# Kernel tuning notes

Hardware: AMD Instinct MI355X
Metric: run time of the kernel (lower is better)

Reference implementation:

```python
import jax, jax.numpy as jnp
import numpy as np

IN_DIM = 128
DIM = 32
N_HEADS = 4
EPS = 1e-5


def setup_inputs() -> dict:
    key = jax.random.key(0)
    ks = jax.random.split(key, 8)
    b, L = 1, 320
    s = 0.02
    return {
        "z": jax.random.normal(ks[0], (b, L, L, IN_DIM), dtype=jnp.float32),
        "ln_g": jnp.ones((IN_DIM,), jnp.float32),
        "ln_b": jnp.zeros((IN_DIM,), jnp.float32),
        "Wqkv": jax.random.normal(ks[1], (IN_DIM, DIM * 3 * N_HEADS), jnp.float32) * s,
        "Wpair": jax.random.normal(ks[2], (IN_DIM, N_HEADS), jnp.float32) * s,
        "Wgate": jax.random.normal(ks[3], (IN_DIM, N_HEADS * DIM), jnp.float32) * s,
        "bgate": jnp.zeros((N_HEADS * DIM,), jnp.float32),
        "Wout": jax.random.normal(ks[4], (N_HEADS * DIM, IN_DIM), jnp.float32) * s,
        "bout": jnp.zeros((IN_DIM,), jnp.float32),
    }


def _layernorm(x, g, b):
    m = jnp.mean(x, axis=-1, keepdims=True)
    v = jnp.mean(jnp.square(x - m), axis=-1, keepdims=True)
    return (x - m) * jax.lax.rsqrt(v + EPS) * g + b


def reference(z, ln_g, ln_b, Wqkv, Wpair, Wgate, bgate, Wout, bout):
    B, L, _, _ = z.shape
    zn = _layernorm(z, ln_g, ln_b)  # [b,i,j,c]
    qkv = zn @ Wqkv                 # [b,i,j,3*h*d]
    q, k, v = jnp.split(qkv, 3, axis=-1)
    rs = lambda t: t.reshape(B, L, L, N_HEADS, DIM)
    q, k, v = rs(q), rs(k), rs(v)
    pair_bias = zn @ Wpair          # [b,i,j,h]
    gate = jax.nn.sigmoid(zn @ Wgate + bgate)  # [b,i,j,h*d]
    scale = DIM ** 0.5
    # row-wise: attend over j within each row r=i
    # scores: [b,r,i,j,h]; bias broadcast over r
    scores = jnp.einsum('brihd,brjhd->brijh', q, k / scale)
    scores = scores + pair_bias[:, None]
    attn = jax.nn.softmax(scores, axis=3)
    out = jnp.einsum('brijh,brjhd->brihd', attn, v)  # [b,r,i,h,d]
    out = out.reshape(B, L, L, N_HEADS * DIM)
    return (gate * out) @ Wout + bout
```

## Files before the change

kernel.cpp:

```cpp
#include <hip/hip_runtime.h>
#include <math.h>


#define LL 320
#define CC 128
#define NPOS (LL*LL)

typedef __attribute__((ext_vector_type(8))) __bf16 bf16x8;
typedef __attribute__((ext_vector_type(4))) __bf16 bf16x4;
typedef __attribute__((ext_vector_type(4))) float f32x4;

#define MFMA16(a,b,c) __builtin_amdgcn_mfma_f32_16x16x32_bf16(a,b,c,0,0,0)

__device__ __forceinline__ int swz(int m, int kc) {
    return m*128 + ((kc ^ (m & 7)) << 3);
}

__global__ __launch_bounds__(128) void k_wprep(
    const float* __restrict__ Wqkv, const float* __restrict__ Wgate,
    const float* __restrict__ Wout, __bf16* __restrict__ wT)
{
    const int n = blockIdx.x, t = threadIdx.x;
    float v;
    if (n < 384)      v = Wqkv[(size_t)t*384 + n] * (n < 128 ? 0.17677669529663687f : 1.f);
    else if (n < 512) v = Wgate[(size_t)t*128 + (n-384)];
    else              v = Wout[(size_t)t*128 + (n-512)];
    wT[(size_t)n*128 + t] = (__bf16)v;
}

__global__ __launch_bounds__(512) void k_ln_proj(
    const float* __restrict__ z, const float* __restrict__ lng, const float* __restrict__ lnb,
    const __bf16* __restrict__ wT, const float* __restrict__ Wpair,
    const float* __restrict__ bgate,
    __bf16* __restrict__ qkvb, __bf16* __restrict__ biasb, __bf16* __restrict__ gateb)
{
    __shared__ __bf16 As[128*128];
    __shared__ __bf16 Bs[128*128];
    const int t = threadIdx.x;
    const int posBase = blockIdx.x * 128;

    {
        const int r0 = t >> 2, q = t & 3;
        const float* zp = z + (size_t)(posBase + r0)*CC + q*32;
        float v[32];
        float s = 0.f, sq = 0.f;
#pragma unroll
        for (int i = 0; i < 8; ++i) {
            float4 f = ((const float4*)zp)[i];
            v[4*i+0]=f.x; v[4*i+1]=f.y; v[4*i+2]=f.z; v[4*i+3]=f.w;
            s  += f.x + f.y + f.z + f.w;
            sq += f.x*f.x + f.y*f.y + f.z*f.z + f.w*f.w;
        }
        s  += __shfl_xor(s, 1);  sq += __shfl_xor(sq, 1);
        s  += __shfl_xor(s, 2);  sq += __shfl_xor(sq, 2);
        const float mean = s * (1.f/128.f);
        const float var  = sq * (1.f/128.f) - mean*mean;
        const float rstd = rsqrtf(var + 1e-5f);
        const float4* g4 = (const float4*)(lng + q*32);
        const float4* b4 = (const float4*)(lnb + q*32);
#pragma unroll
        for (int i = 0; i < 8; ++i) {
            float4 gg = g4[i], bb = b4[i];
            v[4*i+0] = (v[4*i+0]-mean)*rstd*gg.x + bb.x;
            v[4*i+1] = (v[4*i+1]-mean)*rstd*gg.y + bb.y;
            v[4*i+2] = (v[4*i+2]-mean)*rstd*gg.z + bb.z;
            v[4*i+3] = (v[4*i+3]-mean)*rstd*gg.w + bb.w;
        }
#pragma unroll
        for (int i2 = 0; i2 < 8; ++i2) {
            bf16x4 pk;
            pk[0] = (__bf16)v[4*i2+0]; pk[1] = (__bf16)v[4*i2+1];
            pk[2] = (__bf16)v[4*i2+2]; pk[3] = (__bf16)v[4*i2+3];
            *(bf16x4*)&As[swz(r0, q*4 + (i2>>1)) + (i2&1)*4] = pk;
        }
        float pc0=0.f, pc1=0.f, pc2=0.f, pc3=0.f;
#pragma unroll 8
        for (int kk = 0; kk < 32; ++kk) {
            float4 wp = *(const float4*)&Wpair[(q*32 + kk)*4];
            pc0 += v[kk]*wp.x; pc1 += v[kk]*wp.y; pc2 += v[kk]*wp.z; pc3 += v[kk]*wp.w;
        }
        pc0 += __shfl_xor(pc0,1); pc0 += __shfl_xor(pc0,2);
        pc1 += __shfl_xor(pc1,1); pc1 += __shfl_xor(pc1,2);
        pc2 += __shfl_xor(pc2,1); pc2 += __shfl_xor(pc2,2);
        pc3 += __shfl_xor(pc3,1); pc3 += __shfl_xor(pc3,2);
        if (q == 0) {
            biasb[0*(size_t)NPOS + posBase + r0] = (__bf16)pc0;
            biasb[1*(size_t)NPOS + posBase + r0] = (__bf16)pc1;
            biasb[2*(size_t)NPOS + posBase + r0] = (__bf16)pc2;
            biasb[3*(size_t)NPOS + posBase + r0] = (__bf16)pc3;
        }
    }

    const int lane = t & 63, wv = t >> 6;
    const int l15 = lane & 15, quad = lane >> 4;
    const int m0 = wv * 16;
    const int srow = t >> 2, skc0 = (t & 3) * 4;

    for (int ch = 0; ch < 4; ++ch) {
        __syncthreads();
        {
            const __bf16* src = wT + (size_t)(ch*128 + srow)*128;
#pragma unroll
            for (int j = 0; j < 4; ++j)
                *(bf16x8*)&Bs[swz(srow, skc0 + j)] = *(const bf16x8*)(src + (skc0 + j)*8);
        }
        __syncthreads();

        f32x4 acc[8] = {};
#pragma unroll
        for (int kstep = 0; kstep < 4; ++kstep) {
            bf16x8 aA = *(const bf16x8*)&As[swz(m0 + l15, kstep*4 + quad)];
#pragma unroll
            for (int nt = 0; nt < 8; ++nt) {
                bf16x8 bB = *(const bf16x8*)&Bs[swz(nt*16 + l15, kstep*4 + quad)];
                acc[nt] = MFMA16(aA, bB, acc[nt]);
            }
        }

        if (ch < 3) {
#pragma unroll
            for (int reg = 0; reg < 4; ++reg) {
                __bf16* qp = qkvb + (size_t)(posBase + m0 + quad*4 + reg)*384 + ch*128 + l15;
#pragma unroll
                for (int nt = 0; nt < 8; ++nt)
                    qp[nt*16] = (__bf16)acc[nt][reg];
            }
        } else {
#pragma unroll
            for (int reg = 0; reg < 4; ++reg) {
                __bf16* gp = gateb + (size_t)(posBase + m0 + quad*4 + reg)*128 + l15;
#pragma unroll
                for (int nt = 0; nt < 8; ++nt) {
                    float x = acc[nt][reg] + bgate[nt*16 + l15];
                    gp[nt*16] = (__bf16)(1.f/(1.f + __expf(-x)));
                }
            }
        }
    }
}

#define KS_ST 40
#define VT_ST 328
#define PW_ST 40
__global__ __launch_bounds__(320) void k_attn(
    const __bf16* __restrict__ qkvb, const __bf16* __restrict__ biasb,
    const __bf16* __restrict__ gateb, __bf16* __restrict__ attb)
{
    __shared__ __bf16 Ks[320*KS_ST];
    __shared__ __bf16 Vt[32*VT_ST];
    __shared__ __bf16 Pw[5*64*PW_ST];

    const int t = threadIdx.x, wave = t / 64, lane = t & 63;
    const int l15 = lane & 15, quad = lane >> 4;
    const int r = blockIdx.x, h = blockIdx.y;
    const int i0 = wave * 64;
    const size_t rowBase = (size_t)r * LL;

    {
        const __bf16* kp = qkvb + (rowBase + t)*384 + 128 + h*32;
#pragma unroll
        for (int c = 0; c < 4; ++c)
            *(bf16x8*)&Ks[t*KS_ST + c*8] = *(const bf16x8*)(kp + c*8);
#pragma unroll
        for (int c = 0; c < 4; ++c) {
            bf16x8 vv = *(const bf16x8*)(kp + 128 + c*8);
#pragma unroll
            for (int e = 0; e < 8; ++e)
                Vt[(c*8 + e)*VT_ST + t] = vv[e];
        }
    }

    bf16x8 qf[4];
#pragma unroll
    for (int nt = 0; nt < 4; ++nt)
        qf[nt] = *(const bf16x8*)(qkvb + (rowBase + i0 + nt*16 + l15)*384 + h*32 + quad*8);

    __syncthreads();

    f32x4 O[4][2] = {};
    float lp[4] = {0.f,0.f,0.f,0.f};
    __bf16* pw = &Pw[wave*64*PW_ST];
    const __bf16* bbase = biasb + (size_t)h*NPOS;

    for (int j0 = 0; j0 < LL; j0 += 32) {
        const f32x4 zero = {0.f,0.f,0.f,0.f};
        bf16x8 kf[2];
#pragma unroll
        for (int mt = 0; mt < 2; ++mt)
            kf[mt] = *(const bf16x8*)&Ks[(j0 + mt*16 + l15)*KS_ST + quad*8];
        f32x4 st[2][4];
#pragma unroll
        for (int mt = 0; mt < 2; ++mt)
#pragma unroll
            for (int nt = 0; nt < 4; ++nt)
                st[mt][nt] = MFMA16(kf[mt], qf[nt], zero);

#pragma unroll
        for (int nt = 0; nt < 4; ++nt) {
            const size_t bi = (size_t)(i0 + nt*16 + l15)*LL + j0;
#pragma unroll
            for (int mt = 0; mt < 2; ++mt) {
                bf16x4 bb = *(const bf16x4*)(bbase + bi + mt*16 + quad*4);
                bf16x4 pk;
                float rs = 0.f;
#pragma unroll
                for (int reg = 0; reg < 4; ++reg) {
                    float p = __expf(st[mt][nt][reg] + (float)bb[reg]);
                    pk[reg] = (__bf16)p;
                    rs += p;
                }
                lp[nt] += rs;
                *(bf16x4*)&pw[(nt*16 + l15)*PW_ST + mt*16 + quad*4] = pk;
            }
        }

        bf16x8 vf[2];
#pragma unroll
        for (int dt = 0; dt < 2; ++dt)
            vf[dt] = *(const bf16x8*)&Vt[(dt*16 + l15)*VT_ST + j0 + quad*8];
#pragma unroll
        for (int nt = 0; nt < 4; ++nt) {
            bf16x8 pf = *(const bf16x8*)&pw[(nt*16 + l15)*PW_ST + quad*8];
#pragma unroll
            for (int dt = 0; dt < 2; ++dt)
                O[nt][dt] = MFMA16(pf, vf[dt], O[nt][dt]);
        }
    }

#pragma unroll
    for (int nt = 0; nt < 4; ++nt) {
        lp[nt] += __shfl_xor(lp[nt], 16);
        lp[nt] += __shfl_xor(lp[nt], 32);
    }
#pragma unroll
    for (int nt = 0; nt < 4; ++nt) {
#pragma unroll
        for (int reg = 0; reg < 4; ++reg) {
            const float lsum = __shfl(lp[nt], quad*4 + reg);
            const float inv = 1.f / lsum;
            const size_t pos = rowBase + i0 + nt*16 + quad*4 + reg;
#pragma unroll
            for (int dt = 0; dt < 2; ++dt) {
                const int d = dt*16 + l15;
                const float g = (float)gateb[pos*128 + h*32 + d];
                attb[pos*128 + h*32 + d] = (__bf16)(O[nt][dt][reg] * inv * g);
            }
        }
    }
}

__global__ __launch_bounds__(512) void k_out(
    const __bf16* __restrict__ attb, const __bf16* __restrict__ wT,
    const float* __restrict__ bout, float* __restrict__ out)
{
    __shared__ __bf16 As[128*128];
    __shared__ __bf16 Bs[128*128];
    const int t = threadIdx.x;
    const int posBase = blockIdx.x * 128;
    const int srow = t >> 2, skc0 = (t & 3) * 4;

    {
        const __bf16* asrc = attb + (size_t)(posBase + srow)*128;
        const __bf16* bsrc = wT + (size_t)(512 + srow)*128;
#pragma unroll
        for (int j = 0; j < 4; ++j) {
            *(bf16x8*)&As[swz(srow, skc0 + j)] = *(const bf16x8*)(asrc + (skc0 + j)*8);
            *(bf16x8*)&Bs[swz(srow, skc0 + j)] = *(const bf16x8*)(bsrc + (skc0 + j)*8);
        }
    }
    __syncthreads();

    const int lane = t & 63, wv = t >> 6;
    const int l15 = lane & 15, quad = lane >> 4;
    const int m0 = wv * 16;

    f32x4 acc[8] = {};
#pragma unroll
    for (int kstep = 0; kstep < 4; ++kstep) {
        bf16x8 aA = *(const bf16x8*)&As[swz(m0 + l15, kstep*4 + quad)];
#pragma unroll
        for (int nt = 0; nt < 8; ++nt) {
            bf16x8 bB = *(const bf16x8*)&Bs[swz(nt*16 + l15, kstep*4 + quad)];
            acc[nt] = MFMA16(aA, bB, acc[nt]);
        }
    }

#pragma unroll
    for (int reg = 0; reg < 4; ++reg) {
        float* op = out + (size_t)(posBase + m0 + quad*4 + reg)*128 + l15;
#pragma unroll
        for (int nt = 0; nt < 8; ++nt)
            op[nt*16] = acc[nt][reg] + bout[nt*16 + l15];
    }
}

extern "C" void kernel_launch(void* const* d_in, const int* in_sizes, int n_in,
                              void* d_out, int out_size, void* d_ws, size_t ws_size,
                              hipStream_t stream) {
    const float* z     = (const float*)d_in[0];
    const float* ln_g  = (const float*)d_in[1];
    const float* ln_b  = (const float*)d_in[2];
    const float* Wqkv  = (const float*)d_in[3];
    const float* Wpair = (const float*)d_in[4];
    const float* Wgate = (const float*)d_in[5];
    const float* bgate = (const float*)d_in[6];
    const float* Wout  = (const float*)d_in[7];
    const float* bout  = (const float*)d_in[8];
    float* out = (float*)d_out;

    __bf16* qkvb  = (__bf16*)d_ws;
    __bf16* attb  = qkvb  + (size_t)NPOS*384;
    __bf16* wT    = attb  + (size_t)NPOS*128;
    __bf16* gateb = wT    + (size_t)640*128;
    __bf16* biasb = gateb + (size_t)NPOS*128;

    k_wprep<<<640, 128, 0, stream>>>(Wqkv, Wgate, Wout, wT);
    k_ln_proj<<<800, 512, 0, stream>>>(z, ln_g, ln_b, wT, Wpair, bgate, qkvb, biasb, gateb);
    k_attn<<<dim3(320, 4), 320, 0, stream>>>(qkvb, biasb, gateb, attb);
    k_out<<<800, 512, 0, stream>>>(attb, wT, bout, out);
}
```

Before: 295.0 us.

## Pre-swizzle pair bias, fold log2e, stream K from global with prefetch

The projection kernel now writes the pair bias pre-scaled by log2(e) in a fragment-ordered layout, so the attention kernel can load it as one contiguous bf16x8 per tile and use exp2f. The Q pre-scale also absorbs log2(e). The K tile is no longer staged in shared memory; K fragments and bias are read straight from global and prefetched one j-block ahead in registers. The P staging buffer is halved and occupancy is hinted with launch bounds. In exchange the code carries more registers and depends on an intricate index mapping that must match the MFMA fragment layout.

```diff
diff --git a/kernel.cpp b/kernel.cpp
--- a/kernel.cpp
+++ b/kernel.cpp
@@ -22,7 +22,7 @@
 {
     const int n = blockIdx.x, t = threadIdx.x;
     float v;
-    if (n < 384)      v = Wqkv[(size_t)t*384 + n] * (n < 128 ? 0.17677669529663687f : 1.f);
+    if (n < 384)      v = Wqkv[(size_t)t*384 + n] * (n < 128 ? 0.25508635f : 1.f);
     else if (n < 512) v = Wgate[(size_t)t*128 + (n-384)];
     else              v = Wout[(size_t)t*128 + (n-512)];
     wT[(size_t)n*128 + t] = (__bf16)v;
@@ -32,7 +32,7 @@
     const float* __restrict__ z, const float* __restrict__ lng, const float* __restrict__ lnb,
     const __bf16* __restrict__ wT, const float* __restrict__ Wpair,
     const float* __restrict__ bgate,
-    __bf16* __restrict__ qkvb, __bf16* __restrict__ biasb, __bf16* __restrict__ gateb)
+    __bf16* __restrict__ qkvb, __bf16* __restrict__ biasX, __bf16* __restrict__ gateb)
 {
     __shared__ __bf16 As[128*128];
     __shared__ __bf16 Bs[128*128];
@@ -84,10 +84,15 @@
         pc2 += __shfl_xor(pc2,1); pc2 += __shfl_xor(pc2,2);
         pc3 += __shfl_xor(pc3,1); pc3 += __shfl_xor(pc3,2);
         if (q == 0) {
-            biasb[0*(size_t)NPOS + posBase + r0] = (__bf16)pc0;
-            biasb[1*(size_t)NPOS + posBase + r0] = (__bf16)pc1;
-            biasb[2*(size_t)NPOS + posBase + r0] = (__bf16)pc2;
-            biasb[3*(size_t)NPOS + posBase + r0] = (__bf16)pc3;
+            const int p = posBase + r0;
+            const int i = p / 320, j = p - i*320;
+            const int mt = (j >> 4) & 1, qd = (j >> 2) & 3, rg = j & 3;
+            const size_t base = ((size_t)(j >> 5)*320 + i)*32 + qd*8 + mt*4 + rg;
+            const float l2e = 1.4426950408889634f;
+            biasX[0*(size_t)NPOS + base] = (__bf16)(pc0*l2e);
+            biasX[1*(size_t)NPOS + base] = (__bf16)(pc1*l2e);
+            biasX[2*(size_t)NPOS + base] = (__bf16)(pc2*l2e);
+            biasX[3*(size_t)NPOS + base] = (__bf16)(pc3*l2e);
         }
     }
 
@@ -139,16 +144,14 @@
     }
 }
 
-#define KS_ST 40
 #define VT_ST 328
 #define PW_ST 40
-__global__ __launch_bounds__(320) void k_attn(
-    const __bf16* __restrict__ qkvb, const __bf16* __restrict__ biasb,
+__global__ __launch_bounds__(320, 4) void k_attn(
+    const __bf16* __restrict__ qkvb, const __bf16* __restrict__ biasX,
     const __bf16* __restrict__ gateb, __bf16* __restrict__ attb)
 {
-    __shared__ __bf16 Ks[320*KS_ST];
     __shared__ __bf16 Vt[32*VT_ST];
-    __shared__ __bf16 Pw[5*64*PW_ST];
+    __shared__ __bf16 Pw[5][32*PW_ST];
 
     const int t = threadIdx.x, wave = t / 64, lane = t & 63;
     const int l15 = lane & 15, quad = lane >> 4;
@@ -157,13 +160,10 @@
     const size_t rowBase = (size_t)r * LL;
 
     {
-        const __bf16* kp = qkvb + (rowBase + t)*384 + 128 + h*32;
-#pragma unroll
-        for (int c = 0; c < 4; ++c)
-            *(bf16x8*)&Ks[t*KS_ST + c*8] = *(const bf16x8*)(kp + c*8);
+        const __bf16* vp = qkvb + (rowBase + t)*384 + 256 + h*32;
 #pragma unroll
         for (int c = 0; c < 4; ++c) {
-            bf16x8 vv = *(const bf16x8*)(kp + 128 + c*8);
+            bf16x8 vv = *(const bf16x8*)(vp + c*8);
 #pragma unroll
             for (int e = 0; e < 8; ++e)
                 Vt[(c*8 + e)*VT_ST + t] = vv[e];
@@ -175,55 +175,75 @@
     for (int nt = 0; nt < 4; ++nt)
         qf[nt] = *(const bf16x8*)(qkvb + (rowBase + i0 + nt*16 + l15)*384 + h*32 + quad*8);
 
+    const __bf16* kbase = qkvb + rowBase*384 + 128 + h*32 + quad*8;
+    const __bf16* bbase = biasX + (size_t)h*NPOS;
+    const size_t bofs0 = ((size_t)(i0 + l15))*32 + quad*8;
+
+    bf16x8 kf0 = *(const bf16x8*)(kbase + (size_t)(l15     )*384);
+    bf16x8 kf1 = *(const bf16x8*)(kbase + (size_t)(16 + l15)*384);
+    bf16x8 bf[4];
+#pragma unroll
+    for (int nt = 0; nt < 4; ++nt)
+        bf[nt] = *(const bf16x8*)(bbase + bofs0 + nt*512);
+
     __syncthreads();
 
     f32x4 O[4][2] = {};
     float lp[4] = {0.f,0.f,0.f,0.f};
-    __bf16* pw = &Pw[wave*64*PW_ST];
-    const __bf16* bbase = biasb + (size_t)h*NPOS;
+    __bf16* pw = &Pw[wave][0];
 
     for (int j0 = 0; j0 < LL; j0 += 32) {
+        const bf16x8 kc0 = kf0, kc1 = kf1;
+        bf16x8 bc[4] = {bf[0], bf[1], bf[2], bf[3]};
+        if (j0 + 32 < LL) {
+            kf0 = *(const bf16x8*)(kbase + (size_t)(j0 + 32 + l15)*384);
+            kf1 = *(const bf16x8*)(kbase + (size_t)(j0 + 48 + l15)*384);
+            const size_t bo = bofs0 + (size_t)((j0 >> 5) + 1)*10240;
+#pragma unroll
+            for (int nt = 0; nt < 4; ++nt)
+                bf[nt] = *(const bf16x8*)(bbase + bo + nt*512);
+        }
+
         const f32x4 zero = {0.f,0.f,0.f,0.f};
-        bf16x8 kf[2];
-#pragma unroll
-        for (int mt = 0; mt < 2; ++mt)
-            kf[mt] = *(const bf16x8*)&Ks[(j0 + mt*16 + l15)*KS_ST + quad*8];
-        f32x4 st[2][4];
-#pragma unroll
-        for (int mt = 0; mt < 2; ++mt)
-#pragma unroll
-            for (int nt = 0; nt < 4; ++nt)
-                st[mt][nt] = MFMA16(kf[mt], qf[nt], zero);
-
-#pragma unroll
-        for (int nt = 0; nt < 4; ++nt) {
-            const size_t bi = (size_t)(i0 + nt*16 + l15)*LL + j0;
-#pragma unroll
-            for (int mt = 0; mt < 2; ++mt) {
-                bf16x4 bb = *(const bf16x4*)(bbase + bi + mt*16 + quad*4);
-                bf16x4 pk;
+        f32x4 st0[4], st1[4];
+#pragma unroll
+        for (int nt = 0; nt < 4; ++nt) st0[nt] = MFMA16(kc0, qf[nt], zero);
+#pragma unroll
+        for (int nt = 0; nt < 4; ++nt) st1[nt] = MFMA16(kc1, qf[nt], zero);
+
+        bf16x8 vf[2];
+#pragma unroll
+        for (int dt = 0; dt < 2; ++dt)
+            vf[dt] = *(const bf16x8*)&Vt[(dt*16 + l15)*VT_ST + j0 + quad*8];
+
+#pragma unroll
+        for (int s = 0; s < 2; ++s) {
+#pragma unroll
+            for (int u = 0; u < 2; ++u) {
+                const int nt = 2*s + u;
+                bf16x4 pk0, pk1;
                 float rs = 0.f;
 #pragma unroll
                 for (int reg = 0; reg < 4; ++reg) {
-                    float p = __expf(st[mt][nt][reg] + (float)bb[reg]);
-                    pk[reg] = (__bf16)p;
-                    rs += p;
+                    float p = exp2f(st0[nt][reg] + (float)bc[nt][reg]);
+                    pk0[reg] = (__bf16)p;  rs += p;
+                }
+#pragma unroll
+                for (int reg = 0; reg < 4; ++reg) {
+                    float p = exp2f(st1[nt][reg] + (float)bc[nt][4+reg]);
+                    pk1[reg] = (__bf16)p;  rs += p;
                 }
                 lp[nt] += rs;
-                *(bf16x4*)&pw[(nt*16 + l15)*PW_ST + mt*16 + quad*4] = pk;
-            }
-        }
-
-        bf16x8 vf[2];
-#pragma unroll
-        for (int dt = 0; dt < 2; ++dt)
-            vf[dt] = *(const bf16x8*)&Vt[(dt*16 + l15)*VT_ST + j0 + quad*8];
-#pragma unroll
-        for (int nt = 0; nt < 4; ++nt) {
-            bf16x8 pf = *(const bf16x8*)&pw[(nt*16 + l15)*PW_ST + quad*8];
-#pragma unroll
-            for (int dt = 0; dt < 2; ++dt)
-                O[nt][dt] = MFMA16(pf, vf[dt], O[nt][dt]);
+                *(bf16x4*)&pw[(u*16 + l15)*PW_ST + quad*4]      = pk0;
+                *(bf16x4*)&pw[(u*16 + l15)*PW_ST + 16 + quad*4] = pk1;
+            }
+#pragma unroll
+            for (int u = 0; u < 2; ++u) {
+                const int nt = 2*s + u;
+                bf16x8 pf = *(const bf16x8*)&pw[(u*16 + l15)*PW_ST + quad*8];
+                O[nt][0] = MFMA16(pf, vf[0], O[nt][0]);
+                O[nt][1] = MFMA16(pf, vf[1], O[nt][1]);
+            }
         }
     }
 
@@ -239,12 +259,10 @@
             const float lsum = __shfl(lp[nt], quad*4 + reg);
             const float inv = 1.f / lsum;
             const size_t pos = rowBase + i0 + nt*16 + quad*4 + reg;
-#pragma unroll
-            for (int dt = 0; dt < 2; ++dt) {
-                const int d = dt*16 + l15;
-                const float g = (float)gateb[pos*128 + h*32 + d];
-                attb[pos*128 + h*32 + d] = (__bf16)(O[nt][dt][reg] * inv * g);
-            }
+            const __bf16* gp = gateb + pos*128 + h*32 + l15;
+            __bf16* op = attb + pos*128 + h*32 + l15;
+            op[0]  = (__bf16)(O[nt][0][reg] * inv * (float)gp[0]);
+            op[16] = (__bf16)(O[nt][1][reg] * inv * (float)gp[16]);
         }
     }
 }
@@ -312,10 +330,10 @@
     __bf16* attb  = qkvb  + (size_t)NPOS*384;
     __bf16* wT    = attb  + (size_t)NPOS*128;
     __bf16* gateb = wT    + (size_t)640*128;
-    __bf16* biasb = gateb + (size_t)NPOS*128;
+    __bf16* biasX = gateb + (size_t)NPOS*128;
 
     k_wprep<<<640, 128, 0, stream>>>(Wqkv, Wgate, Wout, wT);
-    k_ln_proj<<<800, 512, 0, stream>>>(z, ln_g, ln_b, wT, Wpair, bgate, qkvb, biasb, gateb);
-    k_attn<<<dim3(320, 4), 320, 0, stream>>>(qkvb, biasb, gateb, attb);
+    k_ln_proj<<<800, 512, 0, stream>>>(z, ln_g, ln_b, wT, Wpair, bgate, qkvb, biasX, gateb);
+    k_attn<<<dim3(320, 4), 320, 0, stream>>>(qkvb, biasX, gateb, attb);
     k_out<<<800, 512, 0, stream>>>(attb, wT, bout, out);
 }
```

New measurement: 303.5 us. 1.03x slower.
